# Optimization experiments

Hardware: AMD Instinct MI355X
Metric: run time of the kernel (lower is better)

The kernel has to match this reference:

```python
import jax, jax.numpy as jnp
import numpy as np

B, L, D, P = 2, 2048, 768, 1152
I1, I2 = 2048, 3072
H, HD1, HD2 = 12, 64, 96
NC, NP, ND = 3, 6, 3
EPS, ROPE_BASE = 1e-5, 10000.0
STACK_KEYS = ('wq', 'wk', 'wv', 'wo', 'w1', 'w2', 'w3', 'ln1', 'ln2')


def rope_cache(seq_len, n_elem):
    theta = 1.0 / (ROPE_BASE ** (jnp.arange(0, n_elem, 2, dtype=jnp.float32) / n_elem))
    freqs = jnp.outer(jnp.arange(seq_len, dtype=jnp.float32), theta)
    emb = jnp.concatenate([freqs, freqs], axis=-1)  # [T, n_elem]
    return jnp.cos(emb), jnp.sin(emb)


def apply_rope(x, cos, sin):
    half = x.shape[-1] // 2
    x1, x2 = x[..., :half], x[..., half:]
    return x * cos[None, None] + jnp.concatenate([-x2, x1], axis=-1) * sin[None, None]


def rmsnorm(x, w):
    return x * jax.lax.rsqrt(jnp.mean(x * x, axis=-1, keepdims=True) + EPS) * w


def block(x, p, cos, sin):
    Bx, T, Dm = x.shape
    hd = Dm // H
    h = rmsnorm(x, p['ln1'])
    q = (h @ p['wq']).reshape(Bx, T, H, hd).transpose(0, 2, 1, 3)
    k = (h @ p['wk']).reshape(Bx, T, H, hd).transpose(0, 2, 1, 3)
    v = (h @ p['wv']).reshape(Bx, T, H, hd).transpose(0, 2, 1, 3)
    q, k = apply_rope(q, cos, sin), apply_rope(k, cos, sin)
    scores = jnp.einsum('bhqd,bhkd->bhqk', q, k) / jnp.sqrt(jnp.float32(hd))
    scores = jnp.where(jnp.tril(jnp.ones((T, T), dtype=bool)), scores, -jnp.inf)
    o = jnp.einsum('bhqk,bhkd->bhqd', jax.nn.softmax(scores, axis=-1), v)
    x = x + o.transpose(0, 2, 1, 3).reshape(Bx, T, Dm) @ p['wo']
    h = rmsnorm(x, p['ln2'])
    return x + (jax.nn.silu(h @ p['w1']) * (h @ p['w3'])) @ p['w2']


def stack(x, fl, pre, n_layers, cos, sin):
    for i in range(n_layers):
        p = {k: fl[pre + '_' + k][i] for k in STACK_KEYS}
        x = block(x, p, cos, sin)
    return x


def compressor_trunk(fl, cos, sin):
    h = stack(fl['x'], fl, 'comp', NC, cos, sin)
    h = rmsnorm(h, fl['comp_norm'])
    logits = (jax.nn.silu(h @ fl['router_w1'] + fl['router_b1']) @ fl['router_w2'] + fl['router_b2'])[..., 0]
    probs = jax.nn.sigmoid(logits)
    hard = (probs > 0.5).astype(h.dtype)
    bmask = (probs + jax.lax.stop_gradient(hard - probs)).at[:, 0].set(1.0)  # STE
    return h, bmask


def compute_S(fl):
    cos1, sin1 = rope_cache(fl['x'].shape[1], HD1)
    _, bmask = compressor_trunk(fl, cos1, sin1)
    return int(jnp.max(jnp.sum(bmask, axis=-1)))


def model_forward(fl, S):
    Lx = fl['x'].shape[1]
    cos1, sin1 = rope_cache(Lx, HD1)
    h, bmask = compressor_trunk(fl, cos1, sin1)
    bdet = jax.lax.stop_gradient(bmask)
    counts = jnp.sum(bdet, axis=-1).astype(jnp.int32)  # [B]
    cum = jnp.cumsum(bdet, axis=-1)
    assignment = (cum[:, None, :] == jnp.arange(1, S + 1, dtype=cum.dtype)[None, :, None]).astype(h.dtype)
    select = assignment * bmask[:, None, :]  # [B,S,L] one-hot select, grads via STE
    boundaries = jnp.argsort(1.0 - bdet, axis=-1)[:, :S]  # stable desc sort of 0/1 mask
    xc = jnp.einsum('bsl,bld->bsd', select, h) @ fl['up_w']  # ragged gather as GEMM (as original)
    cos2, sin2 = rope_cache(S, HD2)
    xp = rmsnorm(stack(xc, fl, 'proc', NP, cos2, sin2), fl['proc_norm']) @ fl['down_w']
    # decoder: broadcast each chunk embedding back over its positions
    valid = counts[:, None] > jnp.arange(S)[None, :]
    starts = jnp.where(valid[:, :, None], boundaries[:, :, None], Lx)  # [B,S,1]
    chunk_ids = jnp.sum(jnp.arange(Lx)[None, None, :] >= starts, axis=1) - 1  # [B,L]
    y = jnp.take_along_axis(xp, chunk_ids[..., None], axis=1) + h
    y = stack(y, fl, 'dec', ND, cos1, sin1)
    return rmsnorm(y, fl['dec_norm'])


def setup_inputs():
    ks = iter(jax.random.split(jax.random.key(0), 64))
    def w(*shape):
        return jax.random.normal(next(ks), shape, dtype=jnp.float32) * 0.02
    inp = {'x': jax.random.normal(next(ks), (B, L, D), dtype=jnp.float32)}
    for pre, n, d, it in (('comp', NC, D, I1), ('proc', NP, P, I2), ('dec', ND, D, I1)):
        for nm in ('wq', 'wk', 'wv', 'wo'):
            inp[pre + '_' + nm] = w(n, d, d)
        inp[pre + '_w1'], inp[pre + '_w3'], inp[pre + '_w2'] = w(n, d, it), w(n, d, it), w(n, it, d)
        inp[pre + '_ln1'] = jnp.ones((n, d), jnp.float32)
        inp[pre + '_ln2'] = jnp.ones((n, d), jnp.float32)
        inp[pre + '_norm'] = jnp.ones((d,), jnp.float32)
    inp['router_w1'], inp['router_b1'] = w(D, D), jnp.zeros((D,), jnp.float32)
    inp['router_w2'], inp['router_b2'] = w(D, 1), jnp.zeros((1,), jnp.float32)
    inp['up_w'], inp['down_w'] = w(D, P), w(P, D)
    return inp


def reference(x, comp_wq, comp_wk, comp_wv, comp_wo, comp_w1, comp_w2, comp_w3, comp_ln1, comp_ln2, comp_norm, router_w1, router_b1, router_w2, router_b2, up_w, down_w, proc_wq, proc_wk, proc_wv, proc_wo, proc_w1, proc_w2, proc_w3, proc_ln1, proc_ln2, proc_norm, dec_wq, dec_wk, dec_wv, dec_wo, dec_w1, dec_w2, dec_w3, dec_ln1, dec_ln2, dec_norm):
    fl = dict(locals())  # exactly the forward args
    S = compute_S(fl)  # data-dependent number of chunks (concrete, eager)
    return model_forward(fl, S)
```

## Files before the change

kernel.cpp:

```cpp
#include <hip/hip_runtime.h>
#include <cstdint>

static constexpr int LSEQ = 2048;
static constexpr int NHEAD = 12;

typedef unsigned short u16;
typedef __attribute__((ext_vector_type(8))) short bf16x8;
typedef __attribute__((ext_vector_type(8))) unsigned short u16x8;
typedef __attribute__((ext_vector_type(4))) float f32x4;

#define MFMA16 __builtin_amdgcn_mfma_f32_16x16x32_bf16

union U8cvt { u16 u[8]; bf16x8 v; u16x8 w; };

__device__ __forceinline__ float silu(float a) { return a / (1.f + __expf(-a)); }

__device__ __forceinline__ void splitf(float x, u16& h, u16& l) {
    uint32_t ux = __float_as_uint(x);
    uint32_t uh = (ux + 0x7fffu + ((ux >> 16) & 1u)) >> 16;
    float hf = __uint_as_float(uh << 16);
    float r = x - hf;
    uint32_t ur = __float_as_uint(r);
    uint32_t ul = (ur + 0x7fffu + ((ur >> 16) & 1u)) >> 16;
    h = (u16)uh; l = (u16)ul;
}

__device__ __forceinline__ void gld16(const void* g, void* l) {
    __builtin_amdgcn_global_load_lds((const __attribute__((address_space(1))) void*)g,
                                     (__attribute__((address_space(3))) void*)l, 16, 0, 0);
}

struct SplitEnt { const float* s0; const float* s1; const float* s2;
                  u16* dhi; u16* dlo; int K; int Nper; int nsrc; int bstart; int ilv; };
struct SplitArgs { SplitEnt e[4]; int ne; };

__global__ __launch_bounds__(256)
void wsplit_k(SplitArgs a)
{
    const int blk = blockIdx.x;
    int ti = a.ne - 1;
    for (int i = 1; i < a.ne; ++i) if (blk < a.e[i].bstart) { ti = i - 1; break; }
    const SplitEnt E = a.e[ti];
    const int N = E.Nper * E.nsrc;
    const int u = (blk - E.bstart) * 256 + threadIdx.x;
    const int n = u % N, kb = u / N;
    int which, col;
    if (E.ilv) { which = n & 1; col = n >> 1; }
    else       { which = n / E.Nper; col = n - which * E.Nper; }
    const float* sp = (which == 0 ? E.s0 : which == 1 ? E.s1 : E.s2)
                      + (size_t)(kb * 8) * E.Nper + col;
    U8cvt hh, ll;
#pragma unroll
    for (int j = 0; j < 8; ++j) splitf(sp[(size_t)j * E.Nper], hh.u[j], ll.u[j]);
    *(u16x8*)(E.dhi + (size_t)u * 8) = hh.w;
    *(u16x8*)(E.dlo + (size_t)u * 8) = ll.w;
}

template<bool MASK, bool SWI, int BM>
__global__ __launch_bounds__(256)
void gemm_mfma_k(const u16* __restrict__ Ahi, const u16* __restrict__ Alo,
                 const u16* __restrict__ Bhi, const u16* __restrict__ Blo,
                 const float* __restrict__ Res, float* __restrict__ C,
                 u16* __restrict__ Shi, u16* __restrict__ Slo,
                 int N, int K, const int* __restrict__ dS)
{
    constexpr int MFR = BM / 32;
    constexpr int AI  = BM / 32;
    const int n0 = blockIdx.x * 128;
    const int m0 = blockIdx.y * BM;
    int S = 1 << 30;
    if (MASK) { S = *dS; if ((m0 & (LSEQ - 1)) >= S) return; }

    __shared__ u16 sm[2 * BM * 64 + 16384];
    u16* sAhi = sm;
    u16* sAlo = sm + BM * 64;
    u16* sBhi = sm + 2 * BM * 64;
    u16* sBlo = sBhi + 8192;

    const int t = threadIdx.x;
    const int w = t >> 6, lane = t & 63;
    const int wm = (w >> 1) * (BM / 2), wn = (w & 1) * 64;
    const int l15 = lane & 15, l4 = lane >> 4, l7 = lane & 7;

    const f32x4 zf = {0.f, 0.f, 0.f, 0.f};
    f32x4 acc[MFR][4];
#pragma unroll
    for (int i = 0; i < MFR; ++i)
#pragma unroll
        for (int j = 0; j < 4; ++j) acc[i][j] = zf;

    for (int k0 = 0; k0 < K; k0 += 64) {
        __syncthreads();
#pragma unroll
        for (int i = 0; i < AI; ++i) {
            const int q = i * 256 + t;
            const int mrow = q >> 3;
            const int u = (q & 7) ^ (mrow & 7);
            const size_t goff = (size_t)(m0 + mrow) * K + k0 + u * 8;
            const int lbase = i * 2048 + w * 512;
            gld16(Ahi + goff, (void*)(sAhi + lbase));
            gld16(Alo + goff, (void*)(sAlo + lbase));
        }
#pragma unroll
        for (int i = 0; i < 4; ++i) {
            const int q = i * 256 + t;
            const size_t goff = ((size_t)((k0 >> 3) + (q >> 7)) * N + n0 + (q & 127)) * 8;
            const int lbase = i * 2048 + w * 512;
            gld16(Bhi + goff, (void*)(sBhi + lbase));
            gld16(Blo + goff, (void*)(sBlo + lbase));
        }
        __syncthreads();

#pragma unroll
        for (int kk = 0; kk < 2; ++kk) {
            bf16x8 ah[MFR], al[MFR], bh[4], bl[4];
#pragma unroll
            for (int mf = 0; mf < MFR; ++mf) {
                const int row = wm + mf * 16 + l15;
                const int idx = row * 64 + (((kk * 4 + l4) ^ l7) * 8);
                ah[mf] = *(const bf16x8*)(sAhi + idx);
                al[mf] = *(const bf16x8*)(sAlo + idx);
            }
#pragma unroll
            for (int nf = 0; nf < 4; ++nf) {
                const int idx = ((kk * 4 + l4) * 128 + wn + nf * 16 + l15) * 8;
                bh[nf] = *(const bf16x8*)(sBhi + idx);
                bl[nf] = *(const bf16x8*)(sBlo + idx);
            }
#pragma unroll
            for (int mf = 0; mf < MFR; ++mf)
#pragma unroll
                for (int nf = 0; nf < 4; ++nf) {
                    acc[mf][nf] = MFMA16(ah[mf], bh[nf], acc[mf][nf], 0, 0, 0);
                    acc[mf][nf] = MFMA16(ah[mf], bl[nf], acc[mf][nf], 0, 0, 0);
                    acc[mf][nf] = MFMA16(al[mf], bh[nf], acc[mf][nf], 0, 0, 0);
                }
        }
    }

#pragma unroll
    for (int mf = 0; mf < MFR; ++mf) {
#pragma unroll
        for (int r = 0; r < 4; ++r) {
            const int gr = m0 + wm + mf * 16 + l4 * 4 + r;
            if (MASK && (gr & (LSEQ - 1)) >= S) continue;
#pragma unroll
            for (int nf = 0; nf < 4; ++nf) {
                const int gc = n0 + wn + nf * 16 + l15;
                float v = acc[mf][nf][r];
                if (SWI) {
                    const float o = __shfl_xor(v, 1);
                    if (!(l15 & 1)) {
                        const float rr = silu(v) * o;
                        u16 hh, ll; splitf(rr, hh, ll);
                        const size_t bo = (size_t)gr * (N >> 1) + (gc >> 1);
                        Shi[bo] = hh; Slo[bo] = ll;
                    }
                } else {
                    float vv = v;
                    if (Res) vv += Res[(size_t)gr * N + gc];
                    C[(size_t)gr * N + gc] = vv;
                }
            }
        }
    }
}

template<bool F32OUT, bool SPLITOUT>
__global__ __launch_bounds__(256)
void rmsnorm_k(const float* __restrict__ X, const float* __restrict__ w,
               float* __restrict__ OutF, u16* __restrict__ Ohi, u16* __restrict__ Olo,
               int D, const int* __restrict__ dS)
{
    const int row = blockIdx.x;
    if (dS && (row & (LSEQ - 1)) >= *dS) return;
    const float* xr = X + (size_t)row * D;
    float ss = 0.f;
    for (int d = threadIdx.x; d < D; d += 256) { float v = xr[d]; ss += v * v; }
#pragma unroll
    for (int off = 1; off < 64; off <<= 1) ss += __shfl_xor(ss, off);
    __shared__ float red[4];
    if ((threadIdx.x & 63) == 0) red[threadIdx.x >> 6] = ss;
    __syncthreads();
    const float tot = red[0] + red[1] + red[2] + red[3];
    const float rs = rsqrtf(tot / (float)D + 1e-5f);
    for (int d = threadIdx.x; d < D; d += 256) {
        const float y = xr[d] * rs * w[d];
        if (F32OUT) OutF[(size_t)row * D + d] = y;
        if (SPLITOUT) {
            u16 h, l; splitf(y, h, l);
            Ohi[(size_t)row * D + d] = h;
            Olo[(size_t)row * D + d] = l;
        }
    }
}

__global__ void ropetab_k(float* c1, float* s1, float* c2, float* s2)
{
    const int idx = blockIdx.x * 256 + threadIdx.x;
    if (idx < 2048 * 32) {
        const int pos = idx >> 5, i = idx & 31;
        const float th = powf(10000.f, -(float)(2 * i) / 64.f);
        const float v = (float)pos * th;
        c1[idx] = cosf(v); s1[idx] = sinf(v);
    }
    const int idx2 = idx - 2048 * 32;
    if (idx2 >= 0 && idx2 < 2048 * 48) {
        const int pos = idx2 / 48, i = idx2 - (idx2 / 48) * 48;
        const float th = powf(10000.f, -(float)(2 * i) / 96.f);
        const float v = (float)pos * th;
        c2[idx2] = cosf(v); s2[idx2] = sinf(v);
    }
}

template<int HD>
__global__ __launch_bounds__(256)
void prep_k(float* __restrict__ QKV, u16* __restrict__ Khi, u16* __restrict__ Klo,
            u16* __restrict__ Vthi, u16* __restrict__ Vtlo,
            const float* __restrict__ ct, const float* __restrict__ st,
            int dm, const int* __restrict__ dS)
{
    constexpr int half = HD / 2;
    const int s0 = blockIdx.x * 64;
    if (dS && s0 >= *dS) return;
    const int bh = blockIdx.y;
    const int b = bh / NHEAD, h = bh - b * NHEAD;
    const int qstride = 3 * dm;
    const int t = threadIdx.x;

#pragma unroll
    for (int it = 0; it < 64 * half / 256; ++it) {
        const int e = it * 256 + t;
        const int row = e / half, i = e - row * half;
        const int pos = s0 + row;
        const float c = ct[pos * half + i], sn = st[pos * half + i];
        const size_t g = (size_t)(b * LSEQ + pos) * qstride + h * HD + i;
        float x1 = QKV[g], x2 = QKV[g + half];
        QKV[g] = x1 * c - x2 * sn; QKV[g + half] = x2 * c + x1 * sn;
        const size_t gk = g + dm;
        x1 = QKV[gk]; x2 = QKV[gk + half];
        const float k1 = x1 * c - x2 * sn, k2 = x2 * c + x1 * sn;
        const size_t ko = ((size_t)bh * LSEQ + pos) * HD + i;
        u16 hh, ll;
        splitf(k1, hh, ll); Khi[ko] = hh; Klo[ko] = ll;
        splitf(k2, hh, ll); Khi[ko + half] = hh; Klo[ko + half] = ll;
    }

    __shared__ u16 sh[64][HD], sl[64][HD];
    constexpr int C4 = HD / 4;
#pragma unroll
    for (int it = 0; it < 64 * C4 / 256; ++it) {
        const int q = it * 256 + t;
        const int row = q / C4, c4 = q - row * C4;
        const float4 v = *(const float4*)(QKV + (size_t)(b * LSEQ + s0 + row) * qstride
                                          + 2 * dm + h * HD + c4 * 4);
        u16 hh, ll;
        splitf(v.x, hh, ll); sh[row][c4 * 4 + 0] = hh; sl[row][c4 * 4 + 0] = ll;
        splitf(v.y, hh, ll); sh[row][c4 * 4 + 1] = hh; sl[row][c4 * 4 + 1] = ll;
        splitf(v.z, hh, ll); sh[row][c4 * 4 + 2] = hh; sl[row][c4 * 4 + 2] = ll;
        splitf(v.w, hh, ll); sh[row][c4 * 4 + 3] = hh; sl[row][c4 * 4 + 3] = ll;
    }
    __syncthreads();
    const int s8 = t & 7, d0 = t >> 3;
    for (int d = d0; d < HD; d += 32) {
        U8cvt hh, ll;
#pragma unroll
        for (int j = 0; j < 8; ++j) { hh.u[j] = sh[s8 * 8 + j][d]; ll.u[j] = sl[s8 * 8 + j][d]; }
        const size_t vo = ((size_t)bh * HD + d) * LSEQ + s0 + s8 * 8;
        *(u16x8*)(Vthi + vo) = hh.w;
        *(u16x8*)(Vtlo + vo) = ll.w;
    }
}

template<int HD>
__device__ __forceinline__ int kswz(int u, int r) {
    if constexpr (HD == 64) return u ^ (r & 7);
    else return (u & 12) | ((u & 3) ^ (r & 3));
}

template<int HD, int MF>
__global__ __launch_bounds__(256)
void fattn2_k(const float* __restrict__ QKV, const u16* __restrict__ Khi,
              const u16* __restrict__ Klo, const u16* __restrict__ Vthi,
              const u16* __restrict__ Vtlo, u16* __restrict__ Ohi,
              u16* __restrict__ Olo, float* __restrict__ Pacc,
              float* __restrict__ Pml, int dm, float scale,
              const int* __restrict__ dS)
{
    constexpr int BQ = MF * 64;
    constexpr int NQT = LSEQ / BQ;
    constexpr int NSPL = NQT / 2;
    constexpr int BK = 64;
    constexpr int KG8 = HD / 8;
    constexpr int KO = HD / 32;
    constexpr int NFP = HD / 16;
    constexpr float NEG = -3.0e38f;

    const int x = blockIdx.x;
    int j, half; bool partial;
    if (x < 2 * NSPL) { j = NSPL + (x >> 1); half = x & 1; partial = true; }
    else              { j = x - 2 * NSPL;    half = 0;     partial = false; }
    const int q0 = j * BQ;
    int S = 1 << 30;
    if (dS) { S = *dS; if (q0 >= S) return; }
    const int c0 = (((j + 1) * MF) >> 1) * 64;
    const int kbeg = (partial && half) ? c0 : 0;
    const int kend = partial ? (half ? (j + 1) * BQ : c0) : (j + 1) * BQ;

    const int bh = blockIdx.y;
    const int b = bh / NHEAD, h = bh - b * NHEAD;
    const int qstride = 3 * dm;

    __shared__ u16 smem[2 * BK * HD + 2 * HD * BK + 4 * 2 * MF * 16 * 64];
    u16* sKhi = smem;
    u16* sKlo = sKhi + BK * HD;
    u16* sVhi = sKlo + BK * HD;
    u16* sVlo = sVhi + HD * BK;
    u16* sP   = sVlo + HD * BK;

    const int t = threadIdx.x;
    const int w = t >> 6, lane = t & 63;
    const int l15 = lane & 15, l4 = lane >> 4;
    u16* sPhi = sP + w * (2 * MF * 16 * 64);
    u16* sPlo = sPhi + MF * 16 * 64;

    const int qbase = q0 + w * (MF * 16);

    bf16x8 qh[MF][KO], ql[MF][KO];
#pragma unroll
    for (int mf = 0; mf < MF; ++mf) {
        const float* qp = QKV + (size_t)(b * LSEQ + qbase + mf * 16 + l15) * qstride + h * HD;
#pragma unroll
        for (int ki = 0; ki < KO; ++ki) {
            const float* p = qp + (ki * 4 + l4) * 8;
            U8cvt hh, ll;
#pragma unroll
            for (int jj = 0; jj < 8; ++jj) splitf(p[jj] * scale, hh.u[jj], ll.u[jj]);
            qh[mf][ki] = hh.v; ql[mf][ki] = ll.v;
        }
    }

    float m[MF][4], l[MF][4];
#pragma unroll
    for (int mf = 0; mf < MF; ++mf)
#pragma unroll
        for (int r = 0; r < 4; ++r) { m[mf][r] = NEG; l[mf][r] = 0.f; }
    const f32x4 zf = {0.f, 0.f, 0.f, 0.f};
    f32x4 acc[MF][NFP];
#pragma unroll
    for (int mf = 0; mf < MF; ++mf)
#pragma unroll
        for (int nf = 0; nf < NFP; ++nf) acc[mf][nf] = zf;

    const size_t kbase = (size_t)bh * LSEQ * HD;
    const size_t vbase = (size_t)bh * HD * LSEQ;

    for (int k0 = kbeg; k0 < kend; k0 += BK) {
        __syncthreads();
#pragma unroll
        for (int it = 0; it < BK * KG8 / 256; ++it) {
            const int q = it * 256 + t;
            const int r = q / KG8, u = q - r * KG8;
            const int us = kswz<HD>(u, r);
            const size_t go = kbase + (size_t)(k0 + r) * HD + us * 8;
            gld16(Khi + go, (void*)(sKhi + it * 2048 + w * 512));
            gld16(Klo + go, (void*)(sKlo + it * 2048 + w * 512));
        }
#pragma unroll
        for (int it = 0; it < HD * 8 / 256; ++it) {
            const int q = it * 256 + t;
            const int d = q >> 3, u = q & 7;
            const int us = u ^ (d & 7);
            const size_t go = vbase + (size_t)d * LSEQ + k0 + us * 8;
            gld16(Vthi + go, (void*)(sVhi + it * 2048 + w * 512));
            gld16(Vtlo + go, (void*)(sVlo + it * 2048 + w * 512));
        }
        __syncthreads();

        if (k0 < qbase + MF * 16) {
            f32x4 sc[MF][4];
#pragma unroll
            for (int mf = 0; mf < MF; ++mf)
#pragma unroll
                for (int kf = 0; kf < 4; ++kf) sc[mf][kf] = zf;
            __builtin_amdgcn_s_setprio(1);
#pragma unroll
            for (int kf = 0; kf < 4; ++kf) {
                const int row = kf * 16 + l15;
#pragma unroll
                for (int ki = 0; ki < KO; ++ki) {
                    const int idx = row * HD + kswz<HD>(ki * 4 + l4, row) * 8;
                    const bf16x8 kh = *(const bf16x8*)(sKhi + idx);
                    const bf16x8 kl = *(const bf16x8*)(sKlo + idx);
#pragma unroll
                    for (int mf = 0; mf < MF; ++mf) {
                        sc[mf][kf] = MFMA16(qh[mf][ki], kh, sc[mf][kf], 0, 0, 0);
                        sc[mf][kf] = MFMA16(qh[mf][ki], kl, sc[mf][kf], 0, 0, 0);
                        sc[mf][kf] = MFMA16(ql[mf][ki], kh, sc[mf][kf], 0, 0, 0);
                    }
                }
            }
            __builtin_amdgcn_s_setprio(0);

            if (k0 + 63 > qbase) {
#pragma unroll
                for (int mf = 0; mf < MF; ++mf) {
                    const int qg = qbase + mf * 16 + l4 * 4;
#pragma unroll
                    for (int kf = 0; kf < 4; ++kf) {
                        const int jc = k0 + kf * 16 + l15;
#pragma unroll
                        for (int r = 0; r < 4; ++r)
                            if (jc > qg + r) sc[mf][kf][r] = NEG;
                    }
                }
            }

#pragma unroll
            for (int mf = 0; mf < MF; ++mf) {
                float fac[4];
#pragma unroll
                for (int r = 0; r < 4; ++r) {
                    float mx = fmaxf(fmaxf(sc[mf][0][r], sc[mf][1][r]),
                                     fmaxf(sc[mf][2][r], sc[mf][3][r]));
                    mx = fmaxf(mx, __shfl_xor(mx, 1));
                    mx = fmaxf(mx, __shfl_xor(mx, 2));
                    mx = fmaxf(mx, __shfl_xor(mx, 4));
                    mx = fmaxf(mx, __shfl_xor(mx, 8));
                    const float mn = fmaxf(m[mf][r], mx);
                    fac[r] = __expf(m[mf][r] - mn);
                    float rs = 0.f;
                    float pv[4];
#pragma unroll
                    for (int kf = 0; kf < 4; ++kf) { pv[kf] = __expf(sc[mf][kf][r] - mn); rs += pv[kf]; }
                    rs += __shfl_xor(rs, 1);
                    rs += __shfl_xor(rs, 2);
                    rs += __shfl_xor(rs, 4);
                    rs += __shfl_xor(rs, 8);
                    l[mf][r] = l[mf][r] * fac[r] + rs;
                    m[mf][r] = mn;
                    const int prow = mf * 16 + l4 * 4 + r;
                    const int rx = prow & 7;
#pragma unroll
                    for (int kf = 0; kf < 4; ++kf) {
                        u16 hh, ll; splitf(pv[kf], hh, ll);
                        const int a = prow * 64 + (((kf * 2 + (l15 >> 3)) ^ rx) * 8) + (l15 & 7);
                        sPhi[a] = hh; sPlo[a] = ll;
                    }
                }
#pragma unroll
                for (int nf = 0; nf < NFP; ++nf)
#pragma unroll
                    for (int r = 0; r < 4; ++r) acc[mf][nf][r] *= fac[r];
            }

            bf16x8 ph[MF][2], pl[MF][2];
#pragma unroll
            for (int mf = 0; mf < MF; ++mf)
#pragma unroll
                for (int kk = 0; kk < 2; ++kk) {
                    const int a = (mf * 16 + l15) * 64 + (((kk * 4 + l4) ^ (l15 & 7)) * 8);
                    ph[mf][kk] = *(const bf16x8*)(sPhi + a);
                    pl[mf][kk] = *(const bf16x8*)(sPlo + a);
                }
            __builtin_amdgcn_s_setprio(1);
#pragma unroll
            for (int nf = 0; nf < NFP; ++nf) {
                const int row = nf * 16 + l15;
#pragma unroll
                for (int kk = 0; kk < 2; ++kk) {
                    const int idx = row * 64 + ((kk * 4 + l4) ^ (row & 7)) * 8;
                    const bf16x8 vh = *(const bf16x8*)(sVhi + idx);
                    const bf16x8 vl = *(const bf16x8*)(sVlo + idx);
#pragma unroll
                    for (int mf = 0; mf < MF; ++mf) {
                        acc[mf][nf] = MFMA16(ph[mf][kk], vh, acc[mf][nf], 0, 0, 0);
                        acc[mf][nf] = MFMA16(ph[mf][kk], vl, acc[mf][nf], 0, 0, 0);
                        acc[mf][nf] = MFMA16(pl[mf][kk], vh, acc[mf][nf], 0, 0, 0);
                    }
                }
            }
            __builtin_amdgcn_s_setprio(0);
        }
    }

    if (!partial) {
#pragma unroll
        for (int mf = 0; mf < MF; ++mf)
#pragma unroll
            for (int r = 0; r < 4; ++r) {
                const float rl = 1.f / l[mf][r];
                const size_t ro = (size_t)(b * LSEQ + qbase + mf * 16 + l4 * 4 + r) * dm + h * HD;
#pragma unroll
                for (int nf = 0; nf < NFP; ++nf) {
                    u16 hh, ll; splitf(acc[mf][nf][r] * rl, hh, ll);
                    Ohi[ro + nf * 16 + l15] = hh;
                    Olo[ro + nf * 16 + l15] = ll;
                }
            }
    } else {
        const int pi = (bh * NSPL + (j - NSPL)) * 2 + half;
#pragma unroll
        for (int mf = 0; mf < MF; ++mf)
#pragma unroll
            for (int r = 0; r < 4; ++r) {
                const int row = w * (MF * 16) + mf * 16 + l4 * 4 + r;
                float* pa = Pacc + ((size_t)pi * BQ + row) * HD;
#pragma unroll
                for (int nf = 0; nf < NFP; ++nf)
                    pa[nf * 16 + l15] = acc[mf][nf][r];
                if (l15 == 0) {
                    Pml[((size_t)pi * BQ + row) * 2 + 0] = m[mf][r];
                    Pml[((size_t)pi * BQ + row) * 2 + 1] = l[mf][r];
                }
            }
    }
}

template<int HD, int MF>
__global__ __launch_bounds__(256)
void attn_merge_k(const float* __restrict__ Pacc, const float* __restrict__ Pml,
                  u16* __restrict__ Ohi, u16* __restrict__ Olo,
                  int dm, const int* __restrict__ dS)
{
    constexpr int BQ = MF * 64;
    constexpr int NSPL = (LSEQ / BQ) / 2;
    const int jx = blockIdx.x;
    const int q0 = (NSPL + jx) * BQ;
    if (dS && q0 >= *dS) return;
    const int bh = blockIdx.y;
    const int b = bh / NHEAD, h = bh - b * NHEAD;
    const int pi0 = (bh * NSPL + jx) * 2;
    __shared__ float w0s[BQ], w1s[BQ], invs[BQ];
    const int t = threadIdx.x;
    if (t < BQ) {
        const float m0 = Pml[((size_t)pi0 * BQ + t) * 2];
        const float l0 = Pml[((size_t)pi0 * BQ + t) * 2 + 1];
        const float m1 = Pml[((size_t)(pi0 + 1) * BQ + t) * 2];
        const float l1 = Pml[((size_t)(pi0 + 1) * BQ + t) * 2 + 1];
        const float mm = fmaxf(m0, m1);
        const float a = __expf(m0 - mm), c = __expf(m1 - mm);
        w0s[t] = a; w1s[t] = c; invs[t] = 1.f / (a * l0 + c * l1);
    }
    __syncthreads();
    for (int e = t; e < BQ * HD; e += 256) {
        const int row = e / HD, d = e - row * HD;
        const float a0 = Pacc[((size_t)pi0 * BQ + row) * HD + d];
        const float a1 = Pacc[((size_t)(pi0 + 1) * BQ + row) * HD + d];
        const float o = (w0s[row] * a0 + w1s[row] * a1) * invs[row];
        u16 hh, ll; splitf(o, hh, ll);
        const size_t ro = (size_t)(b * LSEQ + q0 + row) * dm + h * HD + d;
        Ohi[ro] = hh; Olo[ro] = ll;
    }
}

__global__ __launch_bounds__(256)
void router2_k(const float* __restrict__ T, const float* __restrict__ b1,
               const float* __restrict__ w2, const float* __restrict__ b2,
               int* __restrict__ mask)
{
    const int row = blockIdx.x;
    const float* tr = T + (size_t)row * 768;
    float p = 0.f;
    for (int d = threadIdx.x; d < 768; d += 256) {
        const float u = tr[d] + b1[d];
        p += u / (1.f + __expf(-u)) * w2[d];
    }
#pragma unroll
    for (int off = 1; off < 64; off <<= 1) p += __shfl_xor(p, off);
    __shared__ float red[4];
    if ((threadIdx.x & 63) == 0) red[threadIdx.x >> 6] = p;
    __syncthreads();
    if (threadIdx.x == 0) {
        const float logit = red[0] + red[1] + red[2] + red[3] + b2[0];
        mask[row] = ((row & (LSEQ - 1)) == 0 || logit > 0.f) ? 1 : 0;
    }
}

__global__ __launch_bounds__(256)
void scan_k(const int* __restrict__ mask, int* __restrict__ cid,
            int* __restrict__ bnd, int* __restrict__ counts)
{
    const int b = blockIdx.x, t = threadIdx.x;
    const int base = b * LSEQ;
    __shared__ int lds[256];
    int loc[8]; int s = 0;
#pragma unroll
    for (int j = 0; j < 8; ++j) { s += mask[base + t * 8 + j]; loc[j] = s; }
    lds[t] = s;
    __syncthreads();
    for (int off = 1; off < 256; off <<= 1) {
        const int v = (t >= off) ? lds[t - off] : 0;
        __syncthreads();
        lds[t] += v;
        __syncthreads();
    }
    const int excl = lds[t] - s;
#pragma unroll
    for (int j = 0; j < 8; ++j) {
        const int e = t * 8 + j;
        const int c = excl + loc[j];
        cid[base + e] = c - 1;
        if (mask[base + e]) bnd[base + c - 1] = e;
    }
    if (t == 255) counts[b] = lds[255];
}

__global__ void smax_k(const int* __restrict__ counts, int* __restrict__ dS)
{
    if (threadIdx.x == 0 && blockIdx.x == 0) {
        int s = counts[0];
        if (counts[1] > s) s = counts[1];
        dS[0] = s;
    }
}

__global__ __launch_bounds__(256)
void gather_k(const float* __restrict__ H, const int* __restrict__ bnd,
              const int* __restrict__ counts, u16* __restrict__ Ghi, u16* __restrict__ Glo)
{
    const int s = blockIdx.x, b = blockIdx.y;
    const int cnt = counts[b];
    const size_t go = ((size_t)b * LSEQ + s) * 768;
    if (s < cnt) {
        const float* h = H + ((size_t)b * LSEQ + bnd[b * LSEQ + s]) * 768;
        for (int d = threadIdx.x; d < 768; d += 256) {
            u16 hi, lo; splitf(h[d], hi, lo);
            Ghi[go + d] = hi; Glo[go + d] = lo;
        }
    } else {
        for (int d = threadIdx.x; d < 768; d += 256) { Ghi[go + d] = 0; Glo[go + d] = 0; }
    }
}

__global__ __launch_bounds__(256)
void ybuild_k(const float* __restrict__ XP, const float* __restrict__ H,
              const int* __restrict__ cid, float* __restrict__ Y)
{
    const int row = blockIdx.x;
    const int b = row >> 11;
    const int c = cid[row];
    const float* xp = XP + ((size_t)b * LSEQ + c) * 768;
    const float* h = H + (size_t)row * 768;
    float* y = Y + (size_t)row * 768;
    for (int d = threadIdx.x; d < 768; d += 256) y[d] = xp[d] + h[d];
}

extern "C" void kernel_launch(void* const* d_in, const int* in_sizes, int n_in,
                              void* d_out, int out_size, void* d_ws, size_t ws_size,
                              hipStream_t stream)
{
    auto F = [&](int i) { return (const float*)d_in[i]; };

    struct SW { const float *wq, *wk, *wv, *wo, *w1, *w3, *w2, *ln1, *ln2, *nrm; };
    SW comp, proc, dec;
    const float *rw1, *rb1, *rw2, *rb2, *upw, *dnw;

    const bool sig = (in_sizes[11] == 589824);
    if (!sig) {
        comp = { F(1), F(2), F(3), F(4), F(5), F(6), F(7), F(8), F(9), F(10) };
        proc = { F(11), F(12), F(13), F(14), F(15), F(16), F(17), F(18), F(19), F(20) };
        dec  = { F(21), F(22), F(23), F(24), F(25), F(26), F(27), F(28), F(29), F(30) };
        rw1 = F(31); rb1 = F(32); rw2 = F(33); rb2 = F(34); upw = F(35); dnw = F(36);
    } else {
        comp = { F(1), F(2), F(3), F(4), F(5), F(7), F(6), F(8), F(9), F(10) };
        rw1 = F(11); rb1 = F(12); rw2 = F(13); rb2 = F(14); upw = F(15); dnw = F(16);
        proc = { F(17), F(18), F(19), F(20), F(21), F(23), F(22), F(24), F(25), F(26) };
        dec  = { F(27), F(28), F(29), F(30), F(31), F(33), F(32), F(34), F(35), F(36) };
    }

    char* ws = (char*)d_ws;
    size_t off = 0;
    auto alloc = [&](size_t bytes) -> void* {
        void* p = ws + off;
        off = (off + bytes + 255) & ~(size_t)255;
        return p;
    };
    float* X    = (float*)alloc(4096ull * 1152 * 4);
    float* BigF = (float*)alloc(4096ull * 6144 * 4);
    float* HC   = (float*)alloc(4096ull * 768 * 4);
    u16* HNhi   = (u16*)alloc(4096ull * 1152 * 2);
    u16* HNlo   = (u16*)alloc(4096ull * 1152 * 2);
    u16* SWhi   = (u16*)alloc(4096ull * 3072 * 2);
    u16* SWlo   = (u16*)alloc(4096ull * 3072 * 2);
    u16* Khi    = (u16*)alloc(24ull * 2048 * 96 * 2);
    u16* Klo    = (u16*)alloc(24ull * 2048 * 96 * 2);
    u16* Vthi   = (u16*)alloc(24ull * 2048 * 96 * 2);
    u16* Vtlo   = (u16*)alloc(24ull * 2048 * 96 * 2);
    float* Pacc = (float*)alloc(24ull * 16 * 2 * 64 * 96 * 4);
    float* Pml  = (float*)alloc(24ull * 16 * 2 * 64 * 2 * 4);
    u16* qkvPhi = (u16*)alloc(3981312ull * 2);
    u16* qkvPlo = (u16*)alloc(3981312ull * 2);
    u16* woPhi  = (u16*)alloc(1327104ull * 2);
    u16* woPlo  = (u16*)alloc(1327104ull * 2);
    u16* w13Phi = (u16*)alloc(7077888ull * 2);
    u16* w13Plo = (u16*)alloc(7077888ull * 2);
    u16* w2Phi  = (u16*)alloc(3538944ull * 2);
    u16* w2Plo  = (u16*)alloc(3538944ull * 2);
    u16* rw1Phi = (u16*)alloc(589824ull * 2);
    u16* rw1Plo = (u16*)alloc(589824ull * 2);
    u16* upwPhi = (u16*)alloc(884736ull * 2);
    u16* upwPlo = (u16*)alloc(884736ull * 2);
    u16* dnwPhi = (u16*)alloc(884736ull * 2);
    u16* dnwPlo = (u16*)alloc(884736ull * 2);
    int* mask   = (int*)alloc(4096 * 4);
    int* cid    = (int*)alloc(4096 * 4);
    int* bnd    = (int*)alloc(4096 * 4);
    int* cnts   = (int*)alloc(2 * 4);
    int* dS     = (int*)alloc(256);
    float* c1   = (float*)alloc(2048ull * 32 * 4);
    float* s1   = (float*)alloc(2048ull * 32 * 4);
    float* c2   = (float*)alloc(2048ull * 48 * 4);
    float* s2   = (float*)alloc(2048ull * 48 * 4);

    float* QKV = BigF;
    float* T13 = BigF;
    float* XP  = BigF;
    u16* Ohi = SWhi;
    u16* Olo = SWlo;

    hipMemcpyAsync(X, F(0), 4096ull * 768 * 4, hipMemcpyDeviceToDevice, stream);
    ropetab_k<<<640, 256, 0, stream>>>(c1, s1, c2, s2);

    {
        SplitArgs sa{};
        sa.ne = 3;
        sa.e[0] = { rw1, nullptr, nullptr, rw1Phi, rw1Plo, 768, 768, 1, 0, 0 };
        sa.e[1] = { upw, nullptr, nullptr, upwPhi, upwPlo, 768, 1152, 1, 288, 0 };
        sa.e[2] = { dnw, nullptr, nullptr, dnwPhi, dnwPlo, 1152, 768, 1, 720, 0 };
        wsplit_k<<<1152, 256, 0, stream>>>(sa);
    }

    auto gemm = [&](const u16* ahi, const u16* alo, const u16* bhi, const u16* blo,
                    const float* res, float* c, int N, int K, const int* ds) {
        if (N <= 1152) {
            if (ds) gemm_mfma_k<true, false, 64><<<dim3(N / 128, 64), 256, 0, stream>>>(
                        ahi, alo, bhi, blo, res, c, nullptr, nullptr, N, K, ds);
            else    gemm_mfma_k<false, false, 64><<<dim3(N / 128, 64), 256, 0, stream>>>(
                        ahi, alo, bhi, blo, res, c, nullptr, nullptr, N, K, nullptr);
        } else {
            if (ds) gemm_mfma_k<true, false, 128><<<dim3(N / 128, 32), 256, 0, stream>>>(
                        ahi, alo, bhi, blo, res, c, nullptr, nullptr, N, K, ds);
            else    gemm_mfma_k<false, false, 128><<<dim3(N / 128, 32), 256, 0, stream>>>(
                        ahi, alo, bhi, blo, res, c, nullptr, nullptr, N, K, nullptr);
        }
    };
    auto gemmswi = [&](const u16* ahi, const u16* alo, const u16* bhi, const u16* blo,
                       u16* shi, u16* slo, int N, int K, const int* ds) {
        if (ds) gemm_mfma_k<true, true, 128><<<dim3(N / 128, 32), 256, 0, stream>>>(
                    ahi, alo, bhi, blo, nullptr, nullptr, shi, slo, N, K, ds);
        else    gemm_mfma_k<false, true, 128><<<dim3(N / 128, 32), 256, 0, stream>>>(
                    ahi, alo, bhi, blo, nullptr, nullptr, shi, slo, N, K, nullptr);
    };

    auto run_layer = [&](const SW& W, int li, int dm, int ff, int hd,
                         const float* ct, const float* st, const int* ds) {
        const size_t wsz = (size_t)dm * dm;
        const float* wq = W.wq + (size_t)li * wsz;
        const float* wk = W.wk + (size_t)li * wsz;
        const float* wv = W.wv + (size_t)li * wsz;
        const float* wo = W.wo + (size_t)li * wsz;
        const float* w1 = W.w1 + (size_t)li * dm * ff;
        const float* w3 = W.w3 + (size_t)li * dm * ff;
        const float* w2 = W.w2 + (size_t)li * ff * dm;
        const float* ln1 = W.ln1 + (size_t)li * dm;
        const float* ln2 = W.ln2 + (size_t)li * dm;
        const float scale = 1.0f / sqrtf((float)hd);

        {
            const int b0 = dm * 3 * dm / 2048, b1 = dm * dm / 2048, b2 = dm * 2 * ff / 2048,
                      b3 = ff * dm / 2048;
            SplitArgs sa{};
            sa.ne = 4;
            sa.e[0] = { wq, wk, wv, qkvPhi, qkvPlo, dm, dm, 3, 0, 0 };
            sa.e[1] = { wo, nullptr, nullptr, woPhi, woPlo, dm, dm, 1, b0, 0 };
            sa.e[2] = { w1, w3, nullptr, w13Phi, w13Plo, dm, ff, 2, b0 + b1, 1 };
            sa.e[3] = { w2, nullptr, nullptr, w2Phi, w2Plo, ff, dm, 1, b0 + b1 + b2, 0 };
            wsplit_k<<<b0 + b1 + b2 + b3, 256, 0, stream>>>(sa);
        }

        rmsnorm_k<false, true><<<4096, 256, 0, stream>>>(X, ln1, nullptr, HNhi, HNlo, dm, ds);
        gemm(HNhi, HNlo, qkvPhi, qkvPlo, nullptr, QKV, 3 * dm, dm, ds);
        if (hd == 64) {
            prep_k<64><<<dim3(32, 24), 256, 0, stream>>>(QKV, Khi, Klo, Vthi, Vtlo, ct, st, dm, ds);
            fattn2_k<64, 1><<<dim3(48, 24), 256, 0, stream>>>(QKV, Khi, Klo, Vthi, Vtlo, Ohi, Olo, Pacc, Pml, dm, scale, ds);
            attn_merge_k<64, 1><<<dim3(16, 24), 256, 0, stream>>>(Pacc, Pml, Ohi, Olo, dm, ds);
        } else {
            prep_k<96><<<dim3(32, 24), 256, 0, stream>>>(QKV, Khi, Klo, Vthi, Vtlo, ct, st, dm, ds);
            fattn2_k<96, 1><<<dim3(48, 24), 256, 0, stream>>>(QKV, Khi, Klo, Vthi, Vtlo, Ohi, Olo, Pacc, Pml, dm, scale, ds);
            attn_merge_k<96, 1><<<dim3(16, 24), 256, 0, stream>>>(Pacc, Pml, Ohi, Olo, dm, ds);
        }
        gemm(Ohi, Olo, woPhi, woPlo, X, X, dm, dm, ds);
        rmsnorm_k<false, true><<<4096, 256, 0, stream>>>(X, ln2, nullptr, HNhi, HNlo, dm, ds);
        gemmswi(HNhi, HNlo, w13Phi, w13Plo, SWhi, SWlo, 2 * ff, dm, ds);
        gemm(SWhi, SWlo, w2Phi, w2Plo, X, X, dm, ff, ds);
    };

    for (int i = 0; i < 3; ++i) run_layer(comp, i, 768, 2048, 64, c1, s1, nullptr);
    rmsnorm_k<true, true><<<4096, 256, 0, stream>>>(X, comp.nrm, HC, HNhi, HNlo, 768, nullptr);

    gemm(HNhi, HNlo, rw1Phi, rw1Plo, nullptr, T13, 768, 768, nullptr);
    router2_k<<<4096, 256, 0, stream>>>(T13, rb1, rw2, rb2, mask);
    scan_k<<<2, 256, 0, stream>>>(mask, cid, bnd, cnts);
    smax_k<<<1, 64, 0, stream>>>(cnts, dS);

    gather_k<<<dim3(LSEQ, 2), 256, 0, stream>>>(HC, bnd, cnts, HNhi, HNlo);
    gemm(HNhi, HNlo, upwPhi, upwPlo, nullptr, X, 1152, 768, dS);

    for (int i = 0; i < 6; ++i) run_layer(proc, i, 1152, 3072, 96, c2, s2, dS);
    rmsnorm_k<false, true><<<4096, 256, 0, stream>>>(X, proc.nrm, nullptr, HNhi, HNlo, 1152, dS);
    gemm(HNhi, HNlo, dnwPhi, dnwPlo, nullptr, XP, 768, 1152, dS);

    ybuild_k<<<4096, 256, 0, stream>>>(XP, HC, cid, X);
    for (int i = 0; i < 3; ++i) run_layer(dec, i, 768, 2048, 64, c1, s1, nullptr);
    rmsnorm_k<true, false><<<4096, 256, 0, stream>>>(X, dec.nrm, (float*)d_out, nullptr, nullptr, 768, nullptr);
}
```

Before: 4.466 ms.

## Split causal attention KV range into 1-4 chunks by query tile depth

Replaces the two-way KV split for the upper half of query tiles with a graded split: tiles 0-7 run whole, 8-15 split in two, 16-23 in three, 24-31 in four. The launch grows to 80 blocks per head pair. The merge kernel now combines up to four partial (m, l, acc) results. The aim is to even out per-block work under the causal mask so the tail of long tiles shrinks, at the cost of more partial-result traffic in global memory and a heavier merge. The MF template parameter and the per-wave skip check are removed.

```diff
diff --git a/kernel.cpp b/kernel.cpp
--- a/kernel.cpp
+++ b/kernel.cpp
@@ -278,7 +278,13 @@
     else return (u & 12) | ((u & 3) ^ (r & 3));
 }
 
-template<int HD, int MF>
+__device__ __forceinline__ int slot_of(int j, int c) {
+    if (j < 16) return 2 * (j - 8) + c;
+    if (j < 24) return 16 + 3 * (j - 16) + c;
+    return 40 + 4 * (j - 24) + c;
+}
+
+template<int HD>
 __global__ __launch_bounds__(256)
 void fattn2_k(const float* __restrict__ QKV, const u16* __restrict__ Khi,
               const u16* __restrict__ Klo, const u16* __restrict__ Vthi,
@@ -287,9 +293,6 @@
               float* __restrict__ Pml, int dm, float scale,
               const int* __restrict__ dS)
 {
-    constexpr int BQ = MF * 64;
-    constexpr int NQT = LSEQ / BQ;
-    constexpr int NSPL = NQT / 2;
     constexpr int BK = 64;
     constexpr int KG8 = HD / 8;
     constexpr int KO = HD / 32;
@@ -297,21 +300,26 @@
     constexpr float NEG = -3.0e38f;
 
     const int x = blockIdx.x;
-    int j, half; bool partial;
-    if (x < 2 * NSPL) { j = NSPL + (x >> 1); half = x & 1; partial = true; }
-    else              { j = x - 2 * NSPL;    half = 0;     partial = false; }
-    const int q0 = j * BQ;
+    int j, c, nc;
+    if (x < 8)       { j = x;                c = 0;            nc = 1; }
+    else if (x < 24) { j = 8 + ((x - 8) >> 1);  c = (x - 8) & 1;  nc = 2; }
+    else if (x < 48) { j = 16 + (x - 24) / 3;   c = (x - 24) % 3; nc = 3; }
+    else             { j = 24 + ((x - 48) >> 2); c = (x - 48) & 3; nc = 4; }
+    const int q0 = j * 64;
     int S = 1 << 30;
     if (dS) { S = *dS; if (q0 >= S) return; }
-    const int c0 = (((j + 1) * MF) >> 1) * 64;
-    const int kbeg = (partial && half) ? c0 : 0;
-    const int kend = partial ? (half ? (j + 1) * BQ : c0) : (j + 1) * BQ;
+    const int T = j + 1;
+    const int cb = T / nc, crem = T - cb * nc;
+    const int cnt = cb + (c < crem ? 1 : 0);
+    const int st  = c * cb + (c < crem ? c : crem);
+    const int kbeg = st * BK;
+    const int kend = (st + cnt) * BK;
 
     const int bh = blockIdx.y;
     const int b = bh / NHEAD, h = bh - b * NHEAD;
     const int qstride = 3 * dm;
 
-    __shared__ u16 smem[2 * BK * HD + 2 * HD * BK + 4 * 2 * MF * 16 * 64];
+    __shared__ u16 smem[2 * BK * HD + 2 * HD * BK + 4 * 2 * 16 * 64];
     u16* sKhi = smem;
     u16* sKlo = sKhi + BK * HD;
     u16* sVhi = sKlo + BK * HD;
@@ -321,36 +329,31 @@
     const int t = threadIdx.x;
     const int w = t >> 6, lane = t & 63;
     const int l15 = lane & 15, l4 = lane >> 4;
-    u16* sPhi = sP + w * (2 * MF * 16 * 64);
-    u16* sPlo = sPhi + MF * 16 * 64;
-
-    const int qbase = q0 + w * (MF * 16);
-
-    bf16x8 qh[MF][KO], ql[MF][KO];
-#pragma unroll
-    for (int mf = 0; mf < MF; ++mf) {
-        const float* qp = QKV + (size_t)(b * LSEQ + qbase + mf * 16 + l15) * qstride + h * HD;
+    u16* sPhi = sP + w * (2 * 16 * 64);
+    u16* sPlo = sPhi + 16 * 64;
+
+    const int qbase = q0 + w * 16;
+
+    bf16x8 qh[KO], ql[KO];
+    {
+        const float* qp = QKV + (size_t)(b * LSEQ + qbase + l15) * qstride + h * HD;
 #pragma unroll
         for (int ki = 0; ki < KO; ++ki) {
             const float* p = qp + (ki * 4 + l4) * 8;
             U8cvt hh, ll;
 #pragma unroll
             for (int jj = 0; jj < 8; ++jj) splitf(p[jj] * scale, hh.u[jj], ll.u[jj]);
-            qh[mf][ki] = hh.v; ql[mf][ki] = ll.v;
-        }
-    }
-
-    float m[MF][4], l[MF][4];
-#pragma unroll
-    for (int mf = 0; mf < MF; ++mf)
-#pragma unroll
-        for (int r = 0; r < 4; ++r) { m[mf][r] = NEG; l[mf][r] = 0.f; }
+            qh[ki] = hh.v; ql[ki] = ll.v;
+        }
+    }
+
+    float m[4], l[4];
+#pragma unroll
+    for (int r = 0; r < 4; ++r) { m[r] = NEG; l[r] = 0.f; }
     const f32x4 zf = {0.f, 0.f, 0.f, 0.f};
-    f32x4 acc[MF][NFP];
-#pragma unroll
-    for (int mf = 0; mf < MF; ++mf)
-#pragma unroll
-        for (int nf = 0; nf < NFP; ++nf) acc[mf][nf] = zf;
+    f32x4 acc[NFP];
+#pragma unroll
+    for (int nf = 0; nf < NFP; ++nf) acc[nf] = zf;
 
     const size_t kbase = (size_t)bh * LSEQ * HD;
     const size_t vbase = (size_t)bh * HD * LSEQ;
@@ -377,177 +380,173 @@
         }
         __syncthreads();
 
-        if (k0 < qbase + MF * 16) {
-            f32x4 sc[MF][4];
-#pragma unroll
-            for (int mf = 0; mf < MF; ++mf)
-#pragma unroll
-                for (int kf = 0; kf < 4; ++kf) sc[mf][kf] = zf;
-            __builtin_amdgcn_s_setprio(1);
+        f32x4 sc[4];
+#pragma unroll
+        for (int kf = 0; kf < 4; ++kf) sc[kf] = zf;
+        __builtin_amdgcn_s_setprio(1);
+#pragma unroll
+        for (int kf = 0; kf < 4; ++kf) {
+            const int row = kf * 16 + l15;
+#pragma unroll
+            for (int ki = 0; ki < KO; ++ki) {
+                const int idx = row * HD + kswz<HD>(ki * 4 + l4, row) * 8;
+                const bf16x8 kh = *(const bf16x8*)(sKhi + idx);
+                const bf16x8 kl = *(const bf16x8*)(sKlo + idx);
+                sc[kf] = MFMA16(qh[ki], kh, sc[kf], 0, 0, 0);
+                sc[kf] = MFMA16(qh[ki], kl, sc[kf], 0, 0, 0);
+                sc[kf] = MFMA16(ql[ki], kh, sc[kf], 0, 0, 0);
+            }
+        }
+        __builtin_amdgcn_s_setprio(0);
+
+        if (k0 + 63 > qbase) {
+            const int qg = qbase + l4 * 4;
 #pragma unroll
             for (int kf = 0; kf < 4; ++kf) {
-                const int row = kf * 16 + l15;
-#pragma unroll
-                for (int ki = 0; ki < KO; ++ki) {
-                    const int idx = row * HD + kswz<HD>(ki * 4 + l4, row) * 8;
-                    const bf16x8 kh = *(const bf16x8*)(sKhi + idx);
-                    const bf16x8 kl = *(const bf16x8*)(sKlo + idx);
-#pragma unroll
-                    for (int mf = 0; mf < MF; ++mf) {
-                        sc[mf][kf] = MFMA16(qh[mf][ki], kh, sc[mf][kf], 0, 0, 0);
-                        sc[mf][kf] = MFMA16(qh[mf][ki], kl, sc[mf][kf], 0, 0, 0);
-                        sc[mf][kf] = MFMA16(ql[mf][ki], kh, sc[mf][kf], 0, 0, 0);
-                    }
+                const int jc = k0 + kf * 16 + l15;
+#pragma unroll
+                for (int r = 0; r < 4; ++r)
+                    if (jc > qg + r) sc[kf][r] = NEG;
+            }
+        }
+
+        {
+            float fac[4];
+#pragma unroll
+            for (int r = 0; r < 4; ++r) {
+                float mx = fmaxf(fmaxf(sc[0][r], sc[1][r]),
+                                 fmaxf(sc[2][r], sc[3][r]));
+                mx = fmaxf(mx, __shfl_xor(mx, 1));
+                mx = fmaxf(mx, __shfl_xor(mx, 2));
+                mx = fmaxf(mx, __shfl_xor(mx, 4));
+                mx = fmaxf(mx, __shfl_xor(mx, 8));
+                const float mn = fmaxf(m[r], mx);
+                fac[r] = __expf(m[r] - mn);
+                float rs = 0.f;
+                float pv[4];
+#pragma unroll
+                for (int kf = 0; kf < 4; ++kf) { pv[kf] = __expf(sc[kf][r] - mn); rs += pv[kf]; }
+                rs += __shfl_xor(rs, 1);
+                rs += __shfl_xor(rs, 2);
+                rs += __shfl_xor(rs, 4);
+                rs += __shfl_xor(rs, 8);
+                l[r] = l[r] * fac[r] + rs;
+                m[r] = mn;
+                const int prow = l4 * 4 + r;
+                const int rx = prow & 7;
+#pragma unroll
+                for (int kf = 0; kf < 4; ++kf) {
+                    u16 hh, ll; splitf(pv[kf], hh, ll);
+                    const int a = prow * 64 + (((kf * 2 + (l15 >> 3)) ^ rx) * 8) + (l15 & 7);
+                    sPhi[a] = hh; sPlo[a] = ll;
                 }
             }
-            __builtin_amdgcn_s_setprio(0);
-
-            if (k0 + 63 > qbase) {
-#pragma unroll
-                for (int mf = 0; mf < MF; ++mf) {
-                    const int qg = qbase + mf * 16 + l4 * 4;
-#pragma unroll
-                    for (int kf = 0; kf < 4; ++kf) {
-                        const int jc = k0 + kf * 16 + l15;
-#pragma unroll
-                        for (int r = 0; r < 4; ++r)
-                            if (jc > qg + r) sc[mf][kf][r] = NEG;
-                    }
-                }
+#pragma unroll
+            for (int nf = 0; nf < NFP; ++nf)
+#pragma unroll
+                for (int r = 0; r < 4; ++r) acc[nf][r] *= fac[r];
+        }
+
+        bf16x8 ph[2], pl[2];
+#pragma unroll
+        for (int kk = 0; kk < 2; ++kk) {
+            const int a = l15 * 64 + (((kk * 4 + l4) ^ (l15 & 7)) * 8);
+            ph[kk] = *(const bf16x8*)(sPhi + a);
+            pl[kk] = *(const bf16x8*)(sPlo + a);
+        }
+        __builtin_amdgcn_s_setprio(1);
+#pragma unroll
+        for (int nf = 0; nf < NFP; ++nf) {
+            const int row = nf * 16 + l15;
+#pragma unroll
+            for (int kk = 0; kk < 2; ++kk) {
+                const int idx = row * 64 + ((kk * 4 + l4) ^ (row & 7)) * 8;
+                const bf16x8 vh = *(const bf16x8*)(sVhi + idx);
+                const bf16x8 vl = *(const bf16x8*)(sVlo + idx);
+                acc[nf] = MFMA16(ph[kk], vh, acc[nf], 0, 0, 0);
+                acc[nf] = MFMA16(ph[kk], vl, acc[nf], 0, 0, 0);
+                acc[nf] = MFMA16(pl[kk], vh, acc[nf], 0, 0, 0);
             }
-
-#pragma unroll
-            for (int mf = 0; mf < MF; ++mf) {
-                float fac[4];
-#pragma unroll
-                for (int r = 0; r < 4; ++r) {
-                    float mx = fmaxf(fmaxf(sc[mf][0][r], sc[mf][1][r]),
-                                     fmaxf(sc[mf][2][r], sc[mf][3][r]));
-                    mx = fmaxf(mx, __shfl_xor(mx, 1));
-                    mx = fmaxf(mx, __shfl_xor(mx, 2));
-                    mx = fmaxf(mx, __shfl_xor(mx, 4));
-                    mx = fmaxf(mx, __shfl_xor(mx, 8));
-                    const float mn = fmaxf(m[mf][r], mx);
-                    fac[r] = __expf(m[mf][r] - mn);
-                    float rs = 0.f;
-                    float pv[4];
-#pragma unroll
-                    for (int kf = 0; kf < 4; ++kf) { pv[kf] = __expf(sc[mf][kf][r] - mn); rs += pv[kf]; }
-                    rs += __shfl_xor(rs, 1);
-                    rs += __shfl_xor(rs, 2);
-                    rs += __shfl_xor(rs, 4);
-                    rs += __shfl_xor(rs, 8);
-                    l[mf][r] = l[mf][r] * fac[r] + rs;
-                    m[mf][r] = mn;
-                    const int prow = mf * 16 + l4 * 4 + r;
-                    const int rx = prow & 7;
-#pragma unroll
-                    for (int kf = 0; kf < 4; ++kf) {
-                        u16 hh, ll; splitf(pv[kf], hh, ll);
-                        const int a = prow * 64 + (((kf * 2 + (l15 >> 3)) ^ rx) * 8) + (l15 & 7);
-                        sPhi[a] = hh; sPlo[a] = ll;
-                    }
-                }
-#pragma unroll
-                for (int nf = 0; nf < NFP; ++nf)
-#pragma unroll
-                    for (int r = 0; r < 4; ++r) acc[mf][nf][r] *= fac[r];
+        }
+        __builtin_amdgcn_s_setprio(0);
+    }
+
+    if (nc == 1) {
+#pragma unroll
+        for (int r = 0; r < 4; ++r) {
+            const float rl = 1.f / l[r];
+            const size_t ro = (size_t)(b * LSEQ + qbase + l4 * 4 + r) * dm + h * HD;
+#pragma unroll
+            for (int nf = 0; nf < NFP; ++nf) {
+                u16 hh, ll; splitf(acc[nf][r] * rl, hh, ll);
+                Ohi[ro + nf * 16 + l15] = hh;
+                Olo[ro + nf * 16 + l15] = ll;
             }
-
-            bf16x8 ph[MF][2], pl[MF][2];
-#pragma unroll
-            for (int mf = 0; mf < MF; ++mf)
-#pragma unroll
-                for (int kk = 0; kk < 2; ++kk) {
-                    const int a = (mf * 16 + l15) * 64 + (((kk * 4 + l4) ^ (l15 & 7)) * 8);
-                    ph[mf][kk] = *(const bf16x8*)(sPhi + a);
-                    pl[mf][kk] = *(const bf16x8*)(sPlo + a);
-                }
-            __builtin_amdgcn_s_setprio(1);
-#pragma unroll
-            for (int nf = 0; nf < NFP; ++nf) {
-                const int row = nf * 16 + l15;
-#pragma unroll
-                for (int kk = 0; kk < 2; ++kk) {
-                    const int idx = row * 64 + ((kk * 4 + l4) ^ (row & 7)) * 8;
-                    const bf16x8 vh = *(const bf16x8*)(sVhi + idx);
-                    const bf16x8 vl = *(const bf16x8*)(sVlo + idx);
-#pragma unroll
-                    for (int mf = 0; mf < MF; ++mf) {
-                        acc[mf][nf] = MFMA16(ph[mf][kk], vh, acc[mf][nf], 0, 0, 0);
-                        acc[mf][nf] = MFMA16(ph[mf][kk], vl, acc[mf][nf], 0, 0, 0);
-                        acc[mf][nf] = MFMA16(pl[mf][kk], vh, acc[mf][nf], 0, 0, 0);
-                    }
-                }
+        }
+    } else {
+        const int pi = bh * 72 + slot_of(j, c);
+#pragma unroll
+        for (int r = 0; r < 4; ++r) {
+            const int row = w * 16 + l4 * 4 + r;
+            float* pa = Pacc + ((size_t)pi * 64 + row) * HD;
+#pragma unroll
+            for (int nf = 0; nf < NFP; ++nf)
+                pa[nf * 16 + l15] = acc[nf][r];
+            if (l15 == 0) {
+                Pml[((size_t)pi * 64 + row) * 2 + 0] = m[r];
+                Pml[((size_t)pi * 64 + row) * 2 + 1] = l[r];
             }
-            __builtin_amdgcn_s_setprio(0);
-        }
-    }
-
-    if (!partial) {
-#pragma unroll
-        for (int mf = 0; mf < MF; ++mf)
-#pragma unroll
-            for (int r = 0; r < 4; ++r) {
-                const float rl = 1.f / l[mf][r];
-                const size_t ro = (size_t)(b * LSEQ + qbase + mf * 16 + l4 * 4 + r) * dm + h * HD;
-#pragma unroll
-                for (int nf = 0; nf < NFP; ++nf) {
-                    u16 hh, ll; splitf(acc[mf][nf][r] * rl, hh, ll);
-                    Ohi[ro + nf * 16 + l15] = hh;
-                    Olo[ro + nf * 16 + l15] = ll;
-                }
-            }
-    } else {
-        const int pi = (bh * NSPL + (j - NSPL)) * 2 + half;
-#pragma unroll
-        for (int mf = 0; mf < MF; ++mf)
-#pragma unroll
-            for (int r = 0; r < 4; ++r) {
-                const int row = w * (MF * 16) + mf * 16 + l4 * 4 + r;
-                float* pa = Pacc + ((size_t)pi * BQ + row) * HD;
-#pragma unroll
-                for (int nf = 0; nf < NFP; ++nf)
-                    pa[nf * 16 + l15] = acc[mf][nf][r];
-                if (l15 == 0) {
-                    Pml[((size_t)pi * BQ + row) * 2 + 0] = m[mf][r];
-                    Pml[((size_t)pi * BQ + row) * 2 + 1] = l[mf][r];
-                }
-            }
-    }
-}
-
-template<int HD, int MF>
+        }
+    }
+}
+
+template<int HD>
 __global__ __launch_bounds__(256)
 void attn_merge_k(const float* __restrict__ Pacc, const float* __restrict__ Pml,
                   u16* __restrict__ Ohi, u16* __restrict__ Olo,
                   int dm, const int* __restrict__ dS)
 {
-    constexpr int BQ = MF * 64;
-    constexpr int NSPL = (LSEQ / BQ) / 2;
-    const int jx = blockIdx.x;
-    const int q0 = (NSPL + jx) * BQ;
+    const int j = 8 + blockIdx.x;
+    const int q0 = j * 64;
     if (dS && q0 >= *dS) return;
     const int bh = blockIdx.y;
     const int b = bh / NHEAD, h = bh - b * NHEAD;
-    const int pi0 = (bh * NSPL + jx) * 2;
-    __shared__ float w0s[BQ], w1s[BQ], invs[BQ];
+    const int nc = (j < 16) ? 2 : (j < 24) ? 3 : 4;
+    const int pbase = bh * 72 + slot_of(j, 0);
+
+    __shared__ float wsm[4][64], invs[64];
     const int t = threadIdx.x;
-    if (t < BQ) {
-        const float m0 = Pml[((size_t)pi0 * BQ + t) * 2];
-        const float l0 = Pml[((size_t)pi0 * BQ + t) * 2 + 1];
-        const float m1 = Pml[((size_t)(pi0 + 1) * BQ + t) * 2];
-        const float l1 = Pml[((size_t)(pi0 + 1) * BQ + t) * 2 + 1];
-        const float mm = fmaxf(m0, m1);
-        const float a = __expf(m0 - mm), c = __expf(m1 - mm);
-        w0s[t] = a; w1s[t] = c; invs[t] = 1.f / (a * l0 + c * l1);
+    if (t < 64) {
+        float m0, m1, m2 = -3.0e38f, m3 = -3.0e38f;
+        float l0, l1, l2 = 0.f, l3 = 0.f;
+        m0 = Pml[((size_t)(pbase + 0) * 64 + t) * 2];
+        l0 = Pml[((size_t)(pbase + 0) * 64 + t) * 2 + 1];
+        m1 = Pml[((size_t)(pbase + 1) * 64 + t) * 2];
+        l1 = Pml[((size_t)(pbase + 1) * 64 + t) * 2 + 1];
+        if (nc > 2) {
+            m2 = Pml[((size_t)(pbase + 2) * 64 + t) * 2];
+            l2 = Pml[((size_t)(pbase + 2) * 64 + t) * 2 + 1];
+        }
+        if (nc > 3) {
+            m3 = Pml[((size_t)(pbase + 3) * 64 + t) * 2];
+            l3 = Pml[((size_t)(pbase + 3) * 64 + t) * 2 + 1];
+        }
+        const float mm = fmaxf(fmaxf(m0, m1), fmaxf(m2, m3));
+        const float w0 = __expf(m0 - mm);
+        const float w1 = __expf(m1 - mm);
+        const float w2 = (nc > 2) ? __expf(m2 - mm) : 0.f;
+        const float w3 = (nc > 3) ? __expf(m3 - mm) : 0.f;
+        wsm[0][t] = w0; wsm[1][t] = w1; wsm[2][t] = w2; wsm[3][t] = w3;
+        invs[t] = 1.f / (w0 * l0 + w1 * l1 + w2 * l2 + w3 * l3);
     }
     __syncthreads();
-    for (int e = t; e < BQ * HD; e += 256) {
+    for (int e = t; e < 64 * HD; e += 256) {
         const int row = e / HD, d = e - row * HD;
-        const float a0 = Pacc[((size_t)pi0 * BQ + row) * HD + d];
-        const float a1 = Pacc[((size_t)(pi0 + 1) * BQ + row) * HD + d];
-        const float o = (w0s[row] * a0 + w1s[row] * a1) * invs[row];
+        float o = wsm[0][row] * Pacc[((size_t)(pbase + 0) * 64 + row) * HD + d]
+                + wsm[1][row] * Pacc[((size_t)(pbase + 1) * 64 + row) * HD + d];
+        if (nc > 2) o += wsm[2][row] * Pacc[((size_t)(pbase + 2) * 64 + row) * HD + d];
+        if (nc > 3) o += wsm[3][row] * Pacc[((size_t)(pbase + 3) * 64 + row) * HD + d];
+        o *= invs[row];
         u16 hh, ll; splitf(o, hh, ll);
         const size_t ro = (size_t)(b * LSEQ + q0 + row) * dm + h * HD + d;
         Ohi[ro] = hh; Olo[ro] = ll;
@@ -687,8 +686,8 @@
     u16* Klo    = (u16*)alloc(24ull * 2048 * 96 * 2);
     u16* Vthi   = (u16*)alloc(24ull * 2048 * 96 * 2);
     u16* Vtlo   = (u16*)alloc(24ull * 2048 * 96 * 2);
-    float* Pacc = (float*)alloc(24ull * 16 * 2 * 64 * 96 * 4);
-    float* Pml  = (float*)alloc(24ull * 16 * 2 * 64 * 2 * 4);
+    float* Pacc = (float*)alloc(24ull * 72 * 64 * 96 * 4);
+    float* Pml  = (float*)alloc(24ull * 72 * 64 * 2 * 4);
     u16* qkvPhi = (u16*)alloc(3981312ull * 2);
     u16* qkvPlo = (u16*)alloc(3981312ull * 2);
     u16* woPhi  = (u16*)alloc(1327104ull * 2);
@@ -783,12 +782,12 @@
         gemm(HNhi, HNlo, qkvPhi, qkvPlo, nullptr, QKV, 3 * dm, dm, ds);
         if (hd == 64) {
             prep_k<64><<<dim3(32, 24), 256, 0, stream>>>(QKV, Khi, Klo, Vthi, Vtlo, ct, st, dm, ds);
-            fattn2_k<64, 1><<<dim3(48, 24), 256, 0, stream>>>(QKV, Khi, Klo, Vthi, Vtlo, Ohi, Olo, Pacc, Pml, dm, scale, ds);
-            attn_merge_k<64, 1><<<dim3(16, 24), 256, 0, stream>>>(Pacc, Pml, Ohi, Olo, dm, ds);
+            fattn2_k<64><<<dim3(80, 24), 256, 0, stream>>>(QKV, Khi, Klo, Vthi, Vtlo, Ohi, Olo, Pacc, Pml, dm, scale, ds);
+            attn_merge_k<64><<<dim3(24, 24), 256, 0, stream>>>(Pacc, Pml, Ohi, Olo, dm, ds);
         } else {
             prep_k<96><<<dim3(32, 24), 256, 0, stream>>>(QKV, Khi, Klo, Vthi, Vtlo, ct, st, dm, ds);
-            fattn2_k<96, 1><<<dim3(48, 24), 256, 0, stream>>>(QKV, Khi, Klo, Vthi, Vtlo, Ohi, Olo, Pacc, Pml, dm, scale, ds);
-            attn_merge_k<96, 1><<<dim3(16, 24), 256, 0, stream>>>(Pacc, Pml, Ohi, Olo, dm, ds);
+            fattn2_k<96><<<dim3(80, 24), 256, 0, stream>>>(QKV, Khi, Klo, Vthi, Vtlo, Ohi, Olo, Pacc, Pml, dm, scale, ds);
+            attn_merge_k<96><<<dim3(24, 24), 256, 0, stream>>>(Pacc, Pml, Ohi, Olo, dm, ds);
         }
         gemm(Ohi, Olo, woPhi, woPlo, X, X, dm, dm, ds);
         rmsnorm_k<false, true><<<4096, 256, 0, stream>>>(X, ln2, nullptr, HNhi, HNlo, dm, ds);
```

After: 4.423 ms. About the same (-1.0%).
